# Kernel optimization log

Hardware: AMD Instinct MI355X
Metric: run time of the kernel (lower is better)

Reference implementation:

```python
import jax, jax.numpy as jnp
import numpy as np

SIGMA_POS = 0.5
SIGMA_FEAT = 1.0


def setup_inputs() -> dict:
    key = jax.random.key(0)
    ks = jax.random.split(key, 6)
    B, N, M, D, F = 4, 4096, 4096, 3, 64
    return {
        "pos1": jax.random.normal(ks[0], (B, N, D), dtype=jnp.float32),
        "feat1": jax.random.normal(ks[1], (B, N, F), dtype=jnp.float32),
        "w1": jax.random.uniform(ks[2], (B, N, 1), dtype=jnp.float32),
        "pos2": jax.random.normal(ks[3], (B, M, D), dtype=jnp.float32),
        "feat2": jax.random.normal(ks[4], (B, M, F), dtype=jnp.float32),
        "w2": jax.random.uniform(ks[5], (B, M, 1), dtype=jnp.float32),
    }


def reference(pos1, feat1, w1, pos2, feat2, w2):
    # pairwise squared distances via |a|^2 + |b|^2 - 2 a.b  (avoids B,N,M,D tensor)
    sq1 = jnp.sum(pos1 ** 2, axis=-1)  # (B, N)
    sq2 = jnp.sum(pos2 ** 2, axis=-1)  # (B, M)
    cross = jnp.einsum("bnd,bmd->bnm", pos1, pos2)  # (B, N, M)
    pos_dist_sq = sq1[:, :, None] + sq2[:, None, :] - 2.0 * cross
    pos_kernel = jnp.exp(-pos_dist_sq / (2.0 * SIGMA_POS ** 2))
    feat_inner = jnp.einsum("bnf,bmf->bnm", feat1, feat2)  # (B, N, M)
    feat_kernel = jnp.exp(-feat_inner / (2.0 * SIGMA_FEAT ** 2))
    weight_outer = w1 * jnp.swapaxes(w2, 1, 2)  # (B,N,1)*(B,1,M) -> (B,N,M)
    kernel = jnp.sum(pos_kernel * feat_kernel * weight_outer, axis=(1, 2))  # (B,)
    return kernel
```

## Files before the change

kernel.cpp:

```cpp
#include <hip/hip_runtime.h>
#include <stdint.h>


typedef _Float16 f16;
typedef _Float16 v8h __attribute__((ext_vector_type(8)));
typedef _Float16 h4  __attribute__((ext_vector_type(4)));
typedef float    v4f __attribute__((ext_vector_type(4)));

#define L2E 1.4426950408889634f
#define BN 4096
#define KP 96

__global__ __launch_bounds__(256) void prep_kernel(
    const float* __restrict__ pos1, const float* __restrict__ feat1, const float* __restrict__ w1,
    const float* __restrict__ pos2, const float* __restrict__ feat2, const float* __restrict__ w2,
    f16* __restrict__ U1, f16* __restrict__ U2)
{
    int tid  = threadIdx.x;
    int ridx = blockIdx.x * 16 + (tid >> 4);
    int c    = tid & 15;
    int side = ridx >> 14;
    int idx  = ridx & 16383;

    const float* feat = side ? feat2 : feat1;
    f16* U   = side ? U2 : U1;
    float fs = side ? -0.5f * L2E : 1.0f;

    float4 v = ((const float4*)feat)[idx * 16 + c];
    *(h4*)(U + (long)idx * KP + 4 + c * 4) =
        h4{(f16)(v.x * fs), (f16)(v.y * fs), (f16)(v.z * fs), (f16)(v.w * fs)};

    if (c == 0) {
        const float* pos = side ? pos2 : pos1;
        const float* w   = side ? w2   : w1;
        float ps  = side ? 2.0f * L2E : 2.0f;
        float p0 = pos[idx*3+0], p1 = pos[idx*3+1], p2 = pos[idx*3+2];
        float la = __builtin_amdgcn_logf(w[idx]) - 2.0f * L2E * (p0*p0 + p1*p1 + p2*p2);
        la = fmaxf(la, -1000.0f);
        f16   hi = (f16)la;
        f16   lo = (f16)(la - (float)hi);
        *(h4*)(U + (long)idx * KP) = h4{(f16)(p0*ps), (f16)(p1*ps), (f16)(p2*ps), (f16)0.0f};
        *(h4*)(U + (long)idx * KP + 68) =
            side ? h4{(f16)1.0f, (f16)1.0f, hi, lo}
                 : h4{hi, lo, (f16)1.0f, (f16)1.0f};
    } else if (c <= 6) {
        *(h4*)(U + (long)idx * KP + 72 + (c - 1) * 4) =
            h4{(f16)0.0f, (f16)0.0f, (f16)0.0f, (f16)0.0f};
    }
}

__global__ __launch_bounds__(256, 4) void varifold_kernel(
    const f16* __restrict__ U1, const f16* __restrict__ U2,
    float* __restrict__ pw)
{
    int tid = threadIdx.x, wave = tid >> 6, lane = tid & 63;
    int stripe = blockIdx.x, nchunk = blockIdx.y, b = blockIdx.z;
    int l15 = lane & 15, quad = lane >> 4;

    long colr = (long)b*BN + stripe*256 + wave*64;
    long row0 = (long)b*BN + nchunk*256;

    v8h bf[3][4];
    #pragma unroll
    for (int j = 0; j < 4; ++j) {
        const f16* r = U2 + (colr + j*16 + l15) * KP + quad*8;
        bf[0][j] = *(const v8h*)(r);
        bf[1][j] = *(const v8h*)(r + 32);
        bf[2][j] = *(const v8h*)(r + 64);
    }

    const f16* Ab = U1 + (row0 + l15) * KP + quad*8;
    v8h afc[3], afn[3];
    afc[0] = *(const v8h*)(Ab);
    afc[1] = *(const v8h*)(Ab + 32);
    afc[2] = *(const v8h*)(Ab + 64);

    float psum = 0.f;
    #pragma unroll 2
    for (int t = 0; t < 16; ++t) {
        const f16* An = Ab + (t < 15 ? (t+1) : t) * 16 * KP;
        afn[0] = *(const v8h*)(An);
        afn[1] = *(const v8h*)(An + 32);
        afn[2] = *(const v8h*)(An + 64);

        v4f acc[4];
        #pragma unroll
        for (int j = 0; j < 4; ++j) acc[j] = v4f{0.f, 0.f, 0.f, 0.f};
        #pragma unroll
        for (int k = 0; k < 3; ++k)
            #pragma unroll
            for (int j = 0; j < 4; ++j)
                acc[j] = __builtin_amdgcn_mfma_f32_16x16x32_f16(afc[k], bf[k][j], acc[j], 0, 0, 0);

        #pragma unroll
        for (int j = 0; j < 4; ++j) {
            psum += __builtin_amdgcn_exp2f(acc[j][0]);
            psum += __builtin_amdgcn_exp2f(acc[j][1]);
            psum += __builtin_amdgcn_exp2f(acc[j][2]);
            psum += __builtin_amdgcn_exp2f(acc[j][3]);
        }

        afc[0] = afn[0]; afc[1] = afn[1]; afc[2] = afn[2];
    }

    #pragma unroll
    for (int off = 32; off > 0; off >>= 1) psum += __shfl_down(psum, off);
    if (lane == 0)
        pw[(((long)b*16 + nchunk)*16 + stripe)*4 + wave] = psum;
}

__global__ __launch_bounds__(256) void reduce_kernel(
    const float* __restrict__ pw, float* __restrict__ out)
{
    __shared__ float sred[4];
    int b = blockIdx.x, tid = threadIdx.x;
    const float* p = pw + (long)b * 1024;
    float v = p[tid] + p[tid + 256] + p[tid + 512] + p[tid + 768];
    #pragma unroll
    for (int off = 32; off > 0; off >>= 1) v += __shfl_down(v, off);
    if ((tid & 63) == 0) sred[tid >> 6] = v;
    __syncthreads();
    if (tid == 0) out[b] = sred[0] + sred[1] + sred[2] + sred[3];
}

extern "C" void kernel_launch(void* const* d_in, const int* in_sizes, int n_in,
                              void* d_out, int out_size, void* d_ws, size_t ws_size,
                              hipStream_t stream) {
    const float* pos1  = (const float*)d_in[0];
    const float* feat1 = (const float*)d_in[1];
    const float* w1    = (const float*)d_in[2];
    const float* pos2  = (const float*)d_in[3];
    const float* feat2 = (const float*)d_in[4];
    const float* w2    = (const float*)d_in[5];
    float* out = (float*)d_out;

    char* ws = (char*)d_ws;
    f16*   U1  = (f16*)(ws);
    f16*   U2  = (f16*)(ws + 3145728);
    float* pw  = (float*)(ws + 6291456);

    prep_kernel<<<2048, 256, 0, stream>>>(pos1, feat1, w1, pos2, feat2, w2, U1, U2);
    dim3 grid(16, 16, 4);
    varifold_kernel<<<grid, 256, 0, stream>>>(U1, U2, pw);
    reduce_kernel<<<4, 256, 0, stream>>>(pw, out);
}
```

Baseline: 88.21 us.

## Switch to 32x32x16 MFMA tiles and shrink padded K from 96 to 80

Replaces the 16x16x32 MFMA tiling with 32x32x16 MFMAs, so each wave computes two 32x32 output tiles per step over five K-chunks of 16. The padded feature width drops from 96 to 80, removing one third of the zero-padding MFMA work and shrinking the staged half-precision buffers. Each tile's A loads now sit after its MFMAs, and the sum uses two partial accumulators. The 32x32 accumulators use more registers, which may hurt occupancy under the 4-blocks launch bound.

```diff
diff --git a/kernel.cpp b/kernel.cpp
--- a/kernel.cpp
+++ b/kernel.cpp
@@ -3,13 +3,13 @@
 
 
 typedef _Float16 f16;
-typedef _Float16 v8h __attribute__((ext_vector_type(8)));
-typedef _Float16 h4  __attribute__((ext_vector_type(4)));
-typedef float    v4f __attribute__((ext_vector_type(4)));
+typedef _Float16 v8h  __attribute__((ext_vector_type(8)));
+typedef _Float16 h4   __attribute__((ext_vector_type(4)));
+typedef float    v16f __attribute__((ext_vector_type(16)));
 
 #define L2E 1.4426950408889634f
 #define BN 4096
-#define KP 96
+#define KP 80
 
 __global__ __launch_bounds__(256) void prep_kernel(
     const float* __restrict__ pos1, const float* __restrict__ feat1, const float* __restrict__ w1,
@@ -43,7 +43,7 @@
         *(h4*)(U + (long)idx * KP + 68) =
             side ? h4{(f16)1.0f, (f16)1.0f, hi, lo}
                  : h4{hi, lo, (f16)1.0f, (f16)1.0f};
-    } else if (c <= 6) {
+    } else if (c <= 2) {
         *(h4*)(U + (long)idx * KP + 72 + (c - 1) * 4) =
             h4{(f16)0.0f, (f16)0.0f, (f16)0.0f, (f16)0.0f};
     }
@@ -55,53 +55,46 @@
 {
     int tid = threadIdx.x, wave = tid >> 6, lane = tid & 63;
     int stripe = blockIdx.x, nchunk = blockIdx.y, b = blockIdx.z;
-    int l15 = lane & 15, quad = lane >> 4;
+    int l31 = lane & 31, kh = lane >> 5;
 
     long colr = (long)b*BN + stripe*256 + wave*64;
     long row0 = (long)b*BN + nchunk*256;
 
-    v8h bf[3][4];
+    v8h bf[5][2];
     #pragma unroll
-    for (int j = 0; j < 4; ++j) {
-        const f16* r = U2 + (colr + j*16 + l15) * KP + quad*8;
-        bf[0][j] = *(const v8h*)(r);
-        bf[1][j] = *(const v8h*)(r + 32);
-        bf[2][j] = *(const v8h*)(r + 64);
+    for (int j = 0; j < 2; ++j) {
+        const f16* r = U2 + (colr + j*32 + l31) * KP + kh*8;
+        #pragma unroll
+        for (int c = 0; c < 5; ++c) bf[c][j] = *(const v8h*)(r + c*16);
     }
 
-    const f16* Ab = U1 + (row0 + l15) * KP + quad*8;
-    v8h afc[3], afn[3];
-    afc[0] = *(const v8h*)(Ab);
-    afc[1] = *(const v8h*)(Ab + 32);
-    afc[2] = *(const v8h*)(Ab + 64);
+    const f16* Ab = U1 + (row0 + l31) * KP + kh*8;
+    v8h af[5];
+    #pragma unroll
+    for (int c = 0; c < 5; ++c) af[c] = *(const v8h*)(Ab + c*16);
 
-    float psum = 0.f;
+    float ps0 = 0.f, ps1 = 0.f;
     #pragma unroll 2
-    for (int t = 0; t < 16; ++t) {
-        const f16* An = Ab + (t < 15 ? (t+1) : t) * 16 * KP;
-        afn[0] = *(const v8h*)(An);
-        afn[1] = *(const v8h*)(An + 32);
-        afn[2] = *(const v8h*)(An + 64);
+    for (int t = 0; t < 8; ++t) {
+        v16f acc0 = {0.f,0.f,0.f,0.f,0.f,0.f,0.f,0.f,0.f,0.f,0.f,0.f,0.f,0.f,0.f,0.f};
+        v16f acc1 = {0.f,0.f,0.f,0.f,0.f,0.f,0.f,0.f,0.f,0.f,0.f,0.f,0.f,0.f,0.f,0.f};
+        #pragma unroll
+        for (int c = 0; c < 5; ++c) {
+            acc0 = __builtin_amdgcn_mfma_f32_32x32x16_f16(af[c], bf[c][0], acc0, 0, 0, 0);
+            acc1 = __builtin_amdgcn_mfma_f32_32x32x16_f16(af[c], bf[c][1], acc1, 0, 0, 0);
+        }
 
-        v4f acc[4];
+        const f16* An = Ab + (long)((t < 7) ? (t + 1) : t) * 32 * KP;
         #pragma unroll
-        for (int j = 0; j < 4; ++j) acc[j] = v4f{0.f, 0.f, 0.f, 0.f};
-        #pragma unroll
-        for (int k = 0; k < 3; ++k)
-            #pragma unroll
-            for (int j = 0; j < 4; ++j)
-                acc[j] = __builtin_amdgcn_mfma_f32_16x16x32_f16(afc[k], bf[k][j], acc[j], 0, 0, 0);
+        for (int c = 0; c < 5; ++c) af[c] = *(const v8h*)(An + c*16);
 
         #pragma unroll
-        for (int j = 0; j < 4; ++j) {
-            psum += __builtin_amdgcn_exp2f(acc[j][0]);
-            psum += __builtin_amdgcn_exp2f(acc[j][1]);
-            psum += __builtin_amdgcn_exp2f(acc[j][2]);
-            psum += __builtin_amdgcn_exp2f(acc[j][3]);
+        for (int j = 0; j < 16; ++j) {
+            ps0 += __builtin_amdgcn_exp2f(acc0[j]);
+            ps1 += __builtin_amdgcn_exp2f(acc1[j]);
         }
-
-        afc[0] = afn[0]; afc[1] = afn[1]; afc[2] = afn[2];
     }
+    float psum = ps0 + ps1;
 
     #pragma unroll
     for (int off = 32; off > 0; off >>= 1) psum += __shfl_down(psum, off);
@@ -136,8 +129,8 @@
 
     char* ws = (char*)d_ws;
     f16*   U1  = (f16*)(ws);
-    f16*   U2  = (f16*)(ws + 3145728);
-    float* pw  = (float*)(ws + 6291456);
+    f16*   U2  = (f16*)(ws + 2621440);
+    float* pw  = (float*)(ws + 5242880);
 
     prep_kernel<<<2048, 256, 0, stream>>>(pos1, feat1, w1, pos2, feat2, w2, U1, U2);
     dim3 grid(16, 16, 4);
```

New measurement: 92.32 us. +4.7%, slower.
